# Performance work log

Hardware: AMD Instinct MI355X
Metric: run time of the kernel (lower is better)

Reference implementation:

```python
import jax, jax.numpy as jnp
import numpy as np

MODEL_DIM = 1024
NUM_HEADS = 16
DIM_PER_HEAD = MODEL_DIM // NUM_HEADS
LN_EPS = 1e-5


def setup_inputs() -> dict:
    key = jax.random.key(0)
    ks = jax.random.split(key, 5)
    B, S, D = 2, 2048, MODEL_DIM
    scale = 1.0 / np.sqrt(D)
    x = jax.random.normal(ks[0], (B, S, D), dtype=jnp.float32)
    # nn.Linear(bias=False) weights stored as [out, in]; we apply x @ W.T
    w_q = jax.random.normal(ks[1], (D, D), dtype=jnp.float32) * scale
    w_k = jax.random.normal(ks[2], (D, D), dtype=jnp.float32) * scale
    w_v = jax.random.normal(ks[3], (D, D), dtype=jnp.float32) * scale
    w_o = jax.random.normal(ks[4], (D, D), dtype=jnp.float32) * scale
    ln_gamma = jnp.ones((D,), dtype=jnp.float32)
    ln_beta = jnp.zeros((D,), dtype=jnp.float32)
    return {"x": x, "w_q": w_q, "w_k": w_k, "w_v": w_v, "w_o": w_o,
            "ln_gamma": ln_gamma, "ln_beta": ln_beta}


def _layer_norm(x, gamma, beta):
    mu = jnp.mean(x, axis=-1, keepdims=True)
    var = jnp.var(x, axis=-1, keepdims=True)
    return (x - mu) * jax.lax.rsqrt(var + LN_EPS) * gamma + beta


def reference(x, w_q, w_k, w_v, w_o, ln_gamma, ln_beta):
    B, S, D = x.shape
    H, Dh = NUM_HEADS, DIM_PER_HEAD
    residual = x
    # projections (Linear bias=False): x @ W.T
    q = (x @ w_q.T).reshape(B, S, H, Dh).transpose(0, 2, 1, 3)  # [B,H,S,Dh]
    k = (x @ w_k.T).reshape(B, S, H, Dh).transpose(0, 2, 1, 3)
    v = (x @ w_v.T).reshape(B, S, H, Dh).transpose(0, 2, 1, 3)
    scale = Dh ** (-0.5)
    scores = jnp.einsum('bhqd,bhkd->bhqk', q, k) * scale  # [B,H,Sq,Sk]
    # FAITHFUL quirk: nn.Softmax(dim=2) normalizes over the QUERY axis (axis=2)
    attn = jax.nn.softmax(scores, axis=2)
    # dropout is identity in eval mode
    ctx = jnp.einsum('bhqk,bhkd->bhqd', attn, v)  # [B,H,S,Dh]
    ctx = ctx.transpose(0, 2, 1, 3).reshape(B, S, D)
    out = ctx @ w_o.T
    return _layer_norm(residual + out, ln_gamma, ln_beta)
```

## Files before the change

### kernel.cpp

```cpp
#include <hip/hip_runtime.h>
#include <hip/hip_bf16.h>

constexpr int kB   = 2;
constexpr int kS   = 2048;
constexpr int kD   = 1024;
constexpr int kH   = 16;
constexpr int kDh  = 64;
constexpr int kBS  = kB * kS;

typedef __attribute__((ext_vector_type(8))) short short8;
typedef __attribute__((ext_vector_type(4))) float floatx4;

__device__ inline unsigned short f2b(float f) {
    __hip_bfloat16 h = __float2bfloat16(f);
    return *reinterpret_cast<unsigned short*>(&h);
}

__device__ inline float b2f(unsigned short u) {
    union { unsigned u; float f; } cv;
    cv.u = (unsigned)u << 16;
    return cv.f;
}

__device__ inline floatx4 mfma16(short8 a, short8 b, floatx4 c) {
    return __builtin_amdgcn_mfma_f32_16x16x32_bf16(a, b, c, 0, 0, 0);
}

__device__ inline void gload16(const unsigned short* g, unsigned short* l) {
    __builtin_amdgcn_global_load_lds(
        (const __attribute__((address_space(1))) void*)g,
        (__attribute__((address_space(3))) void*)l, 16, 0, 0);
}

__global__ void convert_kernel(const float* __restrict__ x,
                               const float* __restrict__ wq, const float* __restrict__ wk,
                               const float* __restrict__ wv, const float* __restrict__ wo,
                               unsigned short* __restrict__ xb, unsigned short* __restrict__ wb) {
    int gid = blockIdx.x * blockDim.x + threadIdx.x;
    long i4 = (long)gid * 4;
    const float* src;
    unsigned short* dst;
    long off;
    if (i4 < (long)kBS * kD) {
        src = x; dst = xb; off = i4;
    } else {
        long w = i4 - (long)kBS * kD;
        int sel = (int)(w >> 20);
        off = w & 1048575;
        src = (sel == 0) ? wq : (sel == 1) ? wk : (sel == 2) ? wv : wo;
        dst = wb + (long)sel * 1048576;
    }
    float4 v = *(const float4*)(src + off);
    ushort4 o;
    o.x = f2b(v.x); o.y = f2b(v.y); o.z = f2b(v.z); o.w = f2b(v.w);
    *(ushort4*)(dst + off) = o;
}

template <int MODE>
__launch_bounds__(256, 2)
__global__ void gemm_nt(const unsigned short* __restrict__ A,
                        const unsigned short* __restrict__ Bw,
                        void* __restrict__ Cout,
                        const float* __restrict__ resid,
                        int M, int N, int K) {
    __shared__ __align__(16) unsigned short As[128 * 64];
    __shared__ __align__(16) unsigned short Bs[128 * 64];

    const int z  = blockIdx.z;
    const unsigned short* Bp = Bw + (size_t)z * N * K;
    const int m0 = blockIdx.y * 128, n0 = blockIdx.x * 128;
    const int tid  = threadIdx.x;
    const int lane = tid & 63, wv = tid >> 6;
    const int wm = wv >> 1, wn = wv & 1;
    const int quad = lane >> 4, l16 = lane & 15;

    floatx4 acc[4][4] = {};

    const int r0 = lane >> 3;
    const int jc = ((lane & 7) ^ r0) * 8;
    const unsigned short* Ag[4];
    const unsigned short* Bg[4];
    unsigned short* Asd[4];
    unsigned short* Bsd[4];
#pragma unroll
    for (int seg = 0; seg < 4; seg++) {
        const int row = seg * 32 + wv * 8 + r0;
        Ag[seg] = A  + (size_t)(m0 + row) * K + jc;
        Bg[seg] = Bp + (size_t)(n0 + row) * K + jc;
        Asd[seg] = As + (seg * 32 + wv * 8) * 64;
        Bsd[seg] = Bs + (seg * 32 + wv * 8) * 64;
    }

    const int pk0 = (quad ^ (l16 & 7)) * 8;
    const int pk1 = ((4 + quad) ^ (l16 & 7)) * 8;

    for (int k0 = 0; k0 < K; k0 += 64) {
        __syncthreads();
#pragma unroll
        for (int seg = 0; seg < 4; seg++) {
            gload16(Ag[seg] + k0, Asd[seg]);
            gload16(Bg[seg] + k0, Bsd[seg]);
        }
        __syncthreads();

#pragma unroll
        for (int h = 0; h < 2; h++) {
            const int pk = h ? pk1 : pk0;
            short8 af[4], bf[4];
#pragma unroll
            for (int i = 0; i < 4; i++)
                af[i] = *(const short8*)(As + (wm * 64 + i * 16 + l16) * 64 + pk);
#pragma unroll
            for (int j = 0; j < 4; j++)
                bf[j] = *(const short8*)(Bs + (wn * 64 + j * 16 + l16) * 64 + pk);
#pragma unroll
            for (int i = 0; i < 4; i++)
#pragma unroll
                for (int j = 0; j < 4; j++)
                    acc[i][j] = mfma16(af[i], bf[j], acc[i][j]);
        }
    }

#pragma unroll
    for (int i = 0; i < 4; i++)
#pragma unroll
        for (int j = 0; j < 4; j++) {
            const int row = m0 + wm * 64 + i * 16 + quad * 4;
            const int col = n0 + wn * 64 + j * 16 + l16;
#pragma unroll
            for (int r = 0; r < 4; r++) {
                float v = acc[i][j][r];
                if (MODE == 0) {
                    if (z == 0) v *= 0.18033688f;
                    ((unsigned short*)Cout)[(size_t)z * M * N + (size_t)(row + r) * N + col] = f2b(v);
                } else {
                    size_t idx = (size_t)(row + r) * N + col;
                    ((float*)Cout)[idx] = v + resid[idx];
                }
            }
        }
}

__launch_bounds__(256, 4)
__global__ void stats_vt_kernel(const unsigned short* __restrict__ Qb,
                                const unsigned short* __restrict__ Kb,
                                const unsigned short* __restrict__ Vb,
                                unsigned short* __restrict__ VT) {
    __shared__ __align__(16) unsigned short Qs[64 * 68];
    __shared__ float s_inv[128];

    const int id = blockIdx.x;
    const int bh = (id & 7) + 8 * ((id >> 3) & 3);
    const int keyblk = id >> 5;
    const int b = bh >> 4, h = bh & 15;
    const int tid = threadIdx.x, lane = tid & 63, w = tid >> 6;
    const int quad = lane >> 4, l16 = lane & 15;
    const int keybase = keyblk * 128 + w * 32;

    short8 ak[2][2];
#pragma unroll
    for (int s = 0; s < 2; s++) {
        const unsigned short* Krow = Kb + (size_t)(b * kS + keybase + s * 16 + l16) * kD + h * kDh;
        ak[s][0] = *(const short8*)(Krow + quad * 8);
        ak[s][1] = *(const short8*)(Krow + 32 + quad * 8);
    }

    const int r0 = lane >> 3;
    const int jc = ((lane & 7) ^ r0) * 8;
    const unsigned short* Qg[2];
    unsigned short* Ql[2];
#pragma unroll
    for (int seg = 0; seg < 2; seg++) {
        const int row = w * 16 + seg * 8 + r0;
        Qg[seg] = Qb + (size_t)(b * kS + row) * kD + h * kDh + jc;
        Ql[seg] = Qs + (w * 16 + seg * 8) * 64;
    }

    const int pk0 = (quad ^ (l16 & 7)) * 8;
    const int pk1 = ((4 + quad) ^ (l16 & 7)) * 8;

    float lacc[2][4] = {};

    for (int q0 = 0; q0 < kS; q0 += 64) {
        __syncthreads();
#pragma unroll
        for (int seg = 0; seg < 2; seg++)
            gload16(Qg[seg] + (size_t)q0 * kD, Ql[seg]);
        __syncthreads();

#pragma unroll
        for (int c = 0; c < 4; c++) {
            const unsigned short* row = Qs + (c * 16 + l16) * 64;
            short8 bq0 = *(const short8*)(row + pk0);
            short8 bq1 = *(const short8*)(row + pk1);
#pragma unroll
            for (int s = 0; s < 2; s++) {
                floatx4 t = {0.f, 0.f, 0.f, 0.f};
                t = mfma16(ak[s][0], bq0, t);
                t = mfma16(ak[s][1], bq1, t);
#pragma unroll
                for (int r = 0; r < 4; r++)
                    lacc[s][r] += exp2f(t[r]);
            }
        }
    }

#pragma unroll
    for (int off = 1; off <= 8; off <<= 1)
#pragma unroll
        for (int s = 0; s < 2; s++)
#pragma unroll
            for (int r = 0; r < 4; r++)
                lacc[s][r] += __shfl_xor(lacc[s][r], off, 64);

    __syncthreads();
    if (l16 == 0) {
#pragma unroll
        for (int s = 0; s < 2; s++)
#pragma unroll
            for (int r = 0; r < 4; r++)
                s_inv[w * 32 + s * 16 + quad * 4 + r] = 1.0f / lacc[s][r];
    }
    __syncthreads();

    unsigned short* tile = Qs;
#pragma unroll
    for (int g = 0; g < 2; g++) {
        const int kr = tid >> 2, dc = (tid & 3) * 16;
        {
            const float iv = s_inv[g * 64 + kr];
            const unsigned short* src =
                Vb + (size_t)(b * kS + keyblk * 128 + g * 64 + kr) * kD + h * kDh + dc;
            unsigned short vs[16];
            *(uint4*)(vs)     = *(const uint4*)(src);
            *(uint4*)(vs + 8) = *(const uint4*)(src + 8);
#pragma unroll
            for (int i = 0; i < 16; i++)
                tile[kr * 65 + dc + i] = f2b(b2f(vs[i]) * iv);
        }
        __syncthreads();
        {
            const int d = tid >> 2, kc = (tid & 3) * 16;
            unsigned short os[16];
#pragma unroll
            for (int j = 0; j < 16; j++) os[j] = tile[(kc + j) * 65 + d];
            unsigned short* dst =
                VT + (size_t)bh * kDh * kS + (size_t)d * kS + keyblk * 128 + g * 64 + kc;
            *(uint4*)(dst)     = *(uint4*)(os);
            *(uint4*)(dst + 8) = *(uint4*)(os + 8);
        }
        __syncthreads();
    }
}

__launch_bounds__(256, 4)
__global__ void ctx_kernel(const unsigned short* __restrict__ Qb,
                           const unsigned short* __restrict__ Kb,
                           const unsigned short* __restrict__ VT,
                           unsigned short* __restrict__ Ctx) {
    constexpr int LDP = 72;
    __shared__ __align__(16) unsigned short Ks[64 * 64];
    __shared__ __align__(16) unsigned short VTs[64 * 64];
    __shared__ __align__(16) unsigned short Pt[4][16 * LDP];

    const int id = blockIdx.x;
    const int bh = (id & 7) + 8 * ((id >> 3) & 3);
    const int qblk = id >> 5;
    const int b = bh >> 4, h = bh & 15;
    const int tid = threadIdx.x, lane = tid & 63, w = tid >> 6;
    const int quad = lane >> 4, l16 = lane & 15;
    const int qbase = qblk * 64 + w * 16;

    short8 aq0, aq1;
    {
        const unsigned short* Qrow = Qb + (size_t)(b * kS + qbase + l16) * kD + h * kDh;
        aq0 = *(const short8*)(Qrow + quad * 8);
        aq1 = *(const short8*)(Qrow + 32 + quad * 8);
    }
    floatx4 acc[4] = {};

    const unsigned short* Kbase = Kb + (size_t)(b * kS) * kD + h * kDh;
    const unsigned short* VTb   = VT + (size_t)bh * kDh * kS;

    const int r0 = lane >> 3;
    const int jc = ((lane & 7) ^ r0) * 8;
    const unsigned short* Kg[2];
    const unsigned short* Vg[2];
    unsigned short* Kl[2];
    unsigned short* Vl[2];
#pragma unroll
    for (int seg = 0; seg < 2; seg++) {
        const int row = w * 16 + seg * 8 + r0;
        Kg[seg] = Kbase + (size_t)row * kD + jc;
        Vg[seg] = VTb + (size_t)row * kS + jc;
        Kl[seg] = Ks  + (w * 16 + seg * 8) * 64;
        Vl[seg] = VTs + (w * 16 + seg * 8) * 64;
    }

    unsigned short* P = Pt[w];
    unsigned short* pw[4];
#pragma unroll
    for (int c = 0; c < 4; c++)
        pw[c] = P + l16 * LDP + ((c ^ (l16 & 3)) * 16) + quad * 4;
    const unsigned short* pr[2];
#pragma unroll
    for (int h2 = 0; h2 < 2; h2++)
        pr[h2] = P + l16 * LDP + (((h2 * 2 + (quad >> 1)) ^ (l16 & 3)) * 16) + (quad & 1) * 8;

    const int pk0 = (quad ^ (l16 & 7)) * 8;
    const int pk1 = ((4 + quad) ^ (l16 & 7)) * 8;

    for (int k0 = 0; k0 < kS; k0 += 64) {
        __syncthreads();
#pragma unroll
        for (int seg = 0; seg < 2; seg++) {
            gload16(Kg[seg] + (size_t)k0 * kD, Kl[seg]);
            gload16(Vg[seg] + k0, Vl[seg]);
        }
        __syncthreads();

        short8 bk[4][2];
#pragma unroll
        for (int c = 0; c < 4; c++) {
            const unsigned short* row = Ks + (c * 16 + l16) * 64;
            bk[c][0] = *(const short8*)(row + pk0);
            bk[c][1] = *(const short8*)(row + pk1);
        }
        floatx4 sc[4];
#pragma unroll
        for (int c = 0; c < 4; c++) {
            floatx4 t = {0.f, 0.f, 0.f, 0.f};
            t = mfma16(bk[c][0], aq0, t);
            sc[c] = mfma16(bk[c][1], aq1, t);
        }
#pragma unroll
        for (int c = 0; c < 4; c++) {
            union { float f; unsigned u; } e0, e1, e2, e3;
            e0.f = exp2f(sc[c][0]);
            e1.f = exp2f(sc[c][1]);
            e2.f = exp2f(sc[c][2]);
            e3.f = exp2f(sc[c][3]);
            uint2 pk;
            pk.x = (e0.u >> 16) | (e1.u & 0xffff0000u);
            pk.y = (e2.u >> 16) | (e3.u & 0xffff0000u);
            *(uint2*)(pw[c]) = pk;
        }

        short8 bv[4][2];
#pragma unroll
        for (int t = 0; t < 4; t++) {
            const unsigned short* row = VTs + (t * 16 + l16) * 64;
            bv[t][0] = *(const short8*)(row + pk0);
            bv[t][1] = *(const short8*)(row + pk1);
        }
        short8 ap0 = *(const short8*)(pr[0]);
        short8 ap1 = *(const short8*)(pr[1]);
#pragma unroll
        for (int t = 0; t < 4; t++) {
            acc[t] = mfma16(ap0, bv[t][0], acc[t]);
            acc[t] = mfma16(ap1, bv[t][1], acc[t]);
        }
    }

#pragma unroll
    for (int t = 0; t < 4; t++)
#pragma unroll
        for (int r = 0; r < 4; r++)
            Ctx[(size_t)(b * kS + qbase + quad * 4 + r) * kD + h * kDh + t * 16 + l16] =
                f2b(acc[t][r]);
}

__global__ void ln_kernel(const float* __restrict__ R, const float* __restrict__ gamma,
                          const float* __restrict__ beta, float* __restrict__ out) {
    const int row = blockIdx.x;
    const int tid = threadIdx.x;
    const float4 v = ((const float4*)(R + (size_t)row * kD))[tid];
    float s  = v.x + v.y + v.z + v.w;
    float ss = v.x * v.x + v.y * v.y + v.z * v.z + v.w * v.w;
#pragma unroll
    for (int off = 32; off > 0; off >>= 1) {
        s  += __shfl_down(s, off, 64);
        ss += __shfl_down(ss, off, 64);
    }
    __shared__ float ws_s[4], ws_ss[4];
    __shared__ float mu_sh, inv_sh;
    const int lane = tid & 63, w = tid >> 6;
    if (lane == 0) { ws_s[w] = s; ws_ss[w] = ss; }
    __syncthreads();
    if (tid == 0) {
        float S1 = ws_s[0] + ws_s[1] + ws_s[2] + ws_s[3];
        float S2 = ws_ss[0] + ws_ss[1] + ws_ss[2] + ws_ss[3];
        float mu = S1 * (1.0f / kD);
        float var = S2 * (1.0f / kD) - mu * mu;
        mu_sh = mu;
        inv_sh = rsqrtf(var + 1e-5f);
    }
    __syncthreads();
    const float mu = mu_sh, inv = inv_sh;
    const float4 g  = ((const float4*)gamma)[tid];
    const float4 bb = ((const float4*)beta)[tid];
    float4 o;
    o.x = (v.x - mu) * inv * g.x + bb.x;
    o.y = (v.y - mu) * inv * g.y + bb.y;
    o.z = (v.z - mu) * inv * g.z + bb.z;
    o.w = (v.w - mu) * inv * g.w + bb.w;
    ((float4*)(out + (size_t)row * kD))[tid] = o;
}

extern "C" void kernel_launch(void* const* d_in, const int* in_sizes, int n_in,
                              void* d_out, int out_size, void* d_ws, size_t ws_size,
                              hipStream_t stream) {
    const float* x     = (const float*)d_in[0];
    const float* wq    = (const float*)d_in[1];
    const float* wk    = (const float*)d_in[2];
    const float* wv    = (const float*)d_in[3];
    const float* wo    = (const float*)d_in[4];
    const float* gamma = (const float*)d_in[5];
    const float* beta  = (const float*)d_in[6];
    float* out = (float*)d_out;

    char* ws = (char*)d_ws;
    unsigned short* Xb  = (unsigned short*)(ws);
    unsigned short* Wb  = (unsigned short*)(ws + (8u  << 20));
    unsigned short* QKV = (unsigned short*)(ws + (16u << 20));
    unsigned short* Qb  = QKV;
    unsigned short* Kb  = QKV + (size_t)kBS * kD;
    unsigned short* Vb  = QKV + (size_t)2 * kBS * kD;
    unsigned short* Ctx = (unsigned short*)(ws + (40u << 20));
    unsigned short* VT  = (unsigned short*)(ws + (48u << 20));
    float* R            = (float*)(ws + (48u << 20));

    convert_kernel<<<8192, 256, 0, stream>>>(x, wq, wk, wv, wo, Xb, Wb);

    gemm_nt<0><<<dim3(kD / 128, kBS / 128, 3), 256, 0, stream>>>(
        Xb, Wb, QKV, nullptr, kBS, kD, kD);

    stats_vt_kernel<<<512, 256, 0, stream>>>(Qb, Kb, Vb, VT);

    ctx_kernel<<<1024, 256, 0, stream>>>(Qb, Kb, VT, Ctx);

    gemm_nt<1><<<dim3(kD / 128, kBS / 128, 1), 256, 0, stream>>>(
        Ctx, Wb + (size_t)3 * kD * kD, R, x, kBS, kD, kD);

    ln_kernel<<<kBS, 256, 0, stream>>>(R, gamma, beta, out);
}
```

Baseline: 249.7 us.

## Switch attention ctx kernel to 32x32 MFMA with in-register P via permlane swap

Rewrites the attention context kernel to use 32x32x16 bf16 MFMA tiles, so each wave covers 32 queries and each block 128 queries. The grid is halved to 512 blocks. The exponentiated score tile is repacked into the A-operand layout in registers with v_permlane32_swap, which removes the LDS round-trip for P. This halves K/V tile reloads per query and drops the P scratch LDS, at the cost of more registers and fewer blocks and waves in flight (launch bounds lowered to 2).

```diff
diff --git a/kernel.cpp b/kernel.cpp
--- a/kernel.cpp
+++ b/kernel.cpp
@@ -10,6 +10,7 @@
 
 typedef __attribute__((ext_vector_type(8))) short short8;
 typedef __attribute__((ext_vector_type(4))) float floatx4;
+typedef __attribute__((ext_vector_type(16))) float floatx16;
 
 __device__ inline unsigned short f2b(float f) {
     __hip_bfloat16 h = __float2bfloat16(f);
@@ -24,6 +25,16 @@
 
 __device__ inline floatx4 mfma16(short8 a, short8 b, floatx4 c) {
     return __builtin_amdgcn_mfma_f32_16x16x32_bf16(a, b, c, 0, 0, 0);
+}
+
+__device__ inline floatx16 mfma32(short8 a, short8 b, floatx16 c) {
+    return __builtin_amdgcn_mfma_f32_32x32x16_bf16(a, b, c, 0, 0, 0);
+}
+
+__device__ inline unsigned packbf(float a, float b) {
+    union { float f; unsigned u; } x, y;
+    x.f = a; y.f = b;
+    return (x.u >> 16) | (y.u & 0xffff0000u);
 }
 
 __device__ inline void gload16(const unsigned short* g, unsigned short* l) {
@@ -253,31 +264,31 @@
     }
 }
 
-__launch_bounds__(256, 4)
+__launch_bounds__(256, 2)
 __global__ void ctx_kernel(const unsigned short* __restrict__ Qb,
                            const unsigned short* __restrict__ Kb,
                            const unsigned short* __restrict__ VT,
                            unsigned short* __restrict__ Ctx) {
-    constexpr int LDP = 72;
     __shared__ __align__(16) unsigned short Ks[64 * 64];
     __shared__ __align__(16) unsigned short VTs[64 * 64];
-    __shared__ __align__(16) unsigned short Pt[4][16 * LDP];
 
     const int id = blockIdx.x;
     const int bh = (id & 7) + 8 * ((id >> 3) & 3);
     const int qblk = id >> 5;
     const int b = bh >> 4, h = bh & 15;
     const int tid = threadIdx.x, lane = tid & 63, w = tid >> 6;
-    const int quad = lane >> 4, l16 = lane & 15;
-    const int qbase = qblk * 64 + w * 16;
-
-    short8 aq0, aq1;
+    const int l32 = lane & 31, hi = lane >> 5;
+    const int qbase = qblk * 128 + w * 32;
+
+    short8 aq[4];
     {
-        const unsigned short* Qrow = Qb + (size_t)(b * kS + qbase + l16) * kD + h * kDh;
-        aq0 = *(const short8*)(Qrow + quad * 8);
-        aq1 = *(const short8*)(Qrow + 32 + quad * 8);
-    }
-    floatx4 acc[4] = {};
+        const unsigned short* Qrow =
+            Qb + (size_t)(b * kS + qbase + l32) * kD + h * kDh + hi * 8;
+#pragma unroll
+        for (int kq = 0; kq < 4; kq++)
+            aq[kq] = *(const short8*)(Qrow + kq * 16);
+    }
+    floatx16 acc[2] = {};
 
     const unsigned short* Kbase = Kb + (size_t)(b * kS) * kD + h * kDh;
     const unsigned short* VTb   = VT + (size_t)bh * kDh * kS;
@@ -297,18 +308,7 @@
         Vl[seg] = VTs + (w * 16 + seg * 8) * 64;
     }
 
-    unsigned short* P = Pt[w];
-    unsigned short* pw[4];
-#pragma unroll
-    for (int c = 0; c < 4; c++)
-        pw[c] = P + l16 * LDP + ((c ^ (l16 & 3)) * 16) + quad * 4;
-    const unsigned short* pr[2];
-#pragma unroll
-    for (int h2 = 0; h2 < 2; h2++)
-        pr[h2] = P + l16 * LDP + (((h2 * 2 + (quad >> 1)) ^ (l16 & 3)) * 16) + (quad & 1) * 8;
-
-    const int pk0 = (quad ^ (l16 & 7)) * 8;
-    const int pk1 = ((4 + quad) ^ (l16 & 7)) * 8;
+    const int x7 = l32 & 7;
 
     for (int k0 = 0; k0 < kS; k0 += 64) {
         __syncthreads();
@@ -319,55 +319,62 @@
         }
         __syncthreads();
 
-        short8 bk[4][2];
-#pragma unroll
-        for (int c = 0; c < 4; c++) {
-            const unsigned short* row = Ks + (c * 16 + l16) * 64;
-            bk[c][0] = *(const short8*)(row + pk0);
-            bk[c][1] = *(const short8*)(row + pk1);
-        }
-        floatx4 sc[4];
-#pragma unroll
-        for (int c = 0; c < 4; c++) {
-            floatx4 t = {0.f, 0.f, 0.f, 0.f};
-            t = mfma16(bk[c][0], aq0, t);
-            sc[c] = mfma16(bk[c][1], aq1, t);
-        }
-#pragma unroll
-        for (int c = 0; c < 4; c++) {
-            union { float f; unsigned u; } e0, e1, e2, e3;
-            e0.f = exp2f(sc[c][0]);
-            e1.f = exp2f(sc[c][1]);
-            e2.f = exp2f(sc[c][2]);
-            e3.f = exp2f(sc[c][3]);
-            uint2 pk;
-            pk.x = (e0.u >> 16) | (e1.u & 0xffff0000u);
-            pk.y = (e2.u >> 16) | (e3.u & 0xffff0000u);
-            *(uint2*)(pw[c]) = pk;
-        }
-
-        short8 bv[4][2];
-#pragma unroll
-        for (int t = 0; t < 4; t++) {
-            const unsigned short* row = VTs + (t * 16 + l16) * 64;
-            bv[t][0] = *(const short8*)(row + pk0);
-            bv[t][1] = *(const short8*)(row + pk1);
-        }
-        short8 ap0 = *(const short8*)(pr[0]);
-        short8 ap1 = *(const short8*)(pr[1]);
-#pragma unroll
-        for (int t = 0; t < 4; t++) {
-            acc[t] = mfma16(ap0, bv[t][0], acc[t]);
-            acc[t] = mfma16(ap1, bv[t][1], acc[t]);
-        }
-    }
-
-#pragma unroll
-    for (int t = 0; t < 4; t++)
-#pragma unroll
-        for (int r = 0; r < 4; r++)
-            Ctx[(size_t)(b * kS + qbase + quad * 4 + r) * kD + h * kDh + t * 16 + l16] =
-                f2b(acc[t][r]);
+        floatx16 sc[2];
+#pragma unroll
+        for (int s = 0; s < 2; s++) {
+            const unsigned short* arow = Ks + (s * 32 + l32) * 64;
+            floatx16 t = {0.f,0.f,0.f,0.f,0.f,0.f,0.f,0.f,
+                          0.f,0.f,0.f,0.f,0.f,0.f,0.f,0.f};
+#pragma unroll
+            for (int kq = 0; kq < 4; kq++) {
+                short8 af = *(const short8*)(arow + ((2 * kq + hi) ^ x7) * 8);
+                t = mfma32(af, aq[kq], t);
+            }
+            sc[s] = t;
+        }
+
+        short8 pa[4];
+#pragma unroll
+        for (int s = 0; s < 2; s++) {
+            float e[16];
+#pragma unroll
+            for (int r = 0; r < 16; r++) e[r] = exp2f(sc[s][r]);
+            unsigned p0 = packbf(e[0],  e[1]),  p1 = packbf(e[2],  e[3]);
+            unsigned p2 = packbf(e[4],  e[5]),  p3 = packbf(e[6],  e[7]);
+            unsigned p4 = packbf(e[8],  e[9]),  p5 = packbf(e[10], e[11]);
+            unsigned p6 = packbf(e[12], e[13]), p7 = packbf(e[14], e[15]);
+            asm volatile("v_permlane32_swap_b32 %0, %1" : "+v"(p0), "+v"(p2));
+            asm volatile("v_permlane32_swap_b32 %0, %1" : "+v"(p1), "+v"(p3));
+            asm volatile("v_permlane32_swap_b32 %0, %1" : "+v"(p4), "+v"(p6));
+            asm volatile("v_permlane32_swap_b32 %0, %1" : "+v"(p5), "+v"(p7));
+            union { unsigned u[4]; short8 v; } f0, f1;
+            f0.u[0] = p0; f0.u[1] = p1; f0.u[2] = p2; f0.u[3] = p3;
+            f1.u[0] = p4; f1.u[1] = p5; f1.u[2] = p6; f1.u[3] = p7;
+            pa[2 * s]     = f0.v;
+            pa[2 * s + 1] = f1.v;
+        }
+
+#pragma unroll
+        for (int t = 0; t < 2; t++) {
+            const unsigned short* brow = VTs + (t * 32 + l32) * 64;
+#pragma unroll
+            for (int kk = 0; kk < 4; kk++) {
+                short8 bv = *(const short8*)(brow + ((2 * kk + hi) ^ x7) * 8);
+                acc[t] = mfma32(pa[kk], bv, acc[t]);
+            }
+        }
+    }
+
+#pragma unroll
+    for (int t = 0; t < 2; t++)
+#pragma unroll
+        for (int rg = 0; rg < 4; rg++)
+#pragma unroll
+            for (int j = 0; j < 4; j++) {
+                const int q = qbase + rg * 8 + hi * 4 + j;
+                const int d = h * kDh + t * 32 + l32;
+                Ctx[(size_t)(b * kS + q) * kD + d] = f2b(acc[t][rg * 4 + j]);
+            }
 }
 
 __global__ void ln_kernel(const float* __restrict__ R, const float* __restrict__ gamma,
@@ -437,7 +444,7 @@
 
     stats_vt_kernel<<<512, 256, 0, stream>>>(Qb, Kb, Vb, VT);
 
-    ctx_kernel<<<1024, 256, 0, stream>>>(Qb, Kb, VT, Ctx);
+    ctx_kernel<<<512, 256, 0, stream>>>(Qb, Kb, VT, Ctx);
 
     gemm_nt<1><<<dim3(kD / 128, kBS / 128, 1), 256, 0, stream>>>(
         Ctx, Wb + (size_t)3 * kD * kD, R, x, kBS, kD, kD);
```

After: 240.3 us. 3.7% less time.
